# Kernel tuning notes

Hardware: AMD Instinct MI355X
Metric: run time of the kernel (lower is better)

Reference implementation:

```python
import jax, jax.numpy as jnp
import numpy as np
from jax import lax

L, B, S, D, H = 2, 8, 2048, 1024, 1024
LOG_H0 = float(np.log(0.5))  # h0 = g(0) = 0.5


def _log_g(x):
    # log of g(x) = x + 0.5 if x >= 0 else sigmoid(x)
    return jnp.where(x >= 0, jnp.log(jnp.where(x >= 0, x + 0.5, 1.0)), -jax.nn.softplus(-x))


def _mingru_layer(x, Wz, bz, Wh, bh):
    # x: (B,S,D) -> (B,S,H) via log-space heinsen associative scan
    k = jnp.einsum('bsd,hd->bsh', x, Wz) + bz          # gate pre-activation
    log_z = -jax.nn.softplus(-k)                        # log sigmoid(k)
    log_coeffs = -jax.nn.softplus(k)                    # log (1 - sigmoid(k))
    pre_h = jnp.einsum('bsd,hd->bsh', x, Wh) + bh
    log_values = log_z + _log_g(pre_h)                  # log(z * h_tilde)
    Bq = x.shape[0]
    # prepend initial state: coeff 0 (log 1), value log(h0)
    log_coeffs = jnp.pad(log_coeffs, ((0, 0), (1, 0), (0, 0)))
    log_values = jnp.concatenate(
        [jnp.full((Bq, 1, log_values.shape[-1]), LOG_H0, dtype=log_values.dtype), log_values], axis=1)
    a_star = jnp.cumsum(log_coeffs, axis=1)
    log_h = a_star + lax.cumlogsumexp(log_values - a_star, axis=1)
    return jnp.exp(log_h)[:, 1:]


def setup_inputs() -> dict:
    key = jax.random.key(0)
    ks = jax.random.split(key, 5)
    stdv = 1.0 / np.sqrt(D)
    u = lambda k, shp: jax.random.uniform(k, shp, jnp.float32, -stdv, stdv)
    return {
        'x': jax.random.normal(ks[0], (B, S, D), jnp.float32),
        'Wz': u(ks[1], (L, H, D)),
        'bz': u(ks[2], (L, H)),
        'Wh': u(ks[3], (L, H, D)),
        'bh': u(ks[4], (L, H)),
    }


def reference(x, Wz, bz, Wh, bh):
    h = x
    for l in range(Wz.shape[0]):
        h = _mingru_layer(h, Wz[l], bz[l], Wh[l], bh[l])
    return h  # (B,S,H), last layer outputs
```

## Files before the change

### kernel.cpp

```cpp
#include <hip/hip_runtime.h>
#include <hip/hip_bf16.h>


#define L_ 2
#define B_ 8
#define S_ 2048
#define D_ 1024
#define H_ 1024
#define M_ (B_*S_)
#define NC 32
#define CL (S_/NC)

typedef __bf16    bf16x8 __attribute__((ext_vector_type(8)));
typedef float     f32x4  __attribute__((ext_vector_type(4)));
typedef _Float16  h2     __attribute__((ext_vector_type(2)));
typedef _Float16  h4     __attribute__((ext_vector_type(4)));

__device__ __forceinline__ ushort f2bf(float f) {
    union { __hip_bfloat16 h; ushort u; } c;
    c.h = __float2bfloat16(f);
    return c.u;
}

__device__ __forceinline__ void async16(const void* g, void* l) {
    __builtin_amdgcn_global_load_lds(
        (const __attribute__((address_space(1))) unsigned int*)g,
        (__attribute__((address_space(3))) unsigned int*)l, 16, 0, 0);
}

__global__ __launch_bounds__(256) void cast_f32_bf16(const float* __restrict__ in,
                                                     ushort* __restrict__ out, int n4) {
    int i = blockIdx.x * 256 + threadIdx.x;
    if (i >= n4) return;
    float4 v = ((const float4*)in)[i];
    ushort4 o;
    o.x = f2bf(v.x); o.y = f2bf(v.y); o.z = f2bf(v.z); o.w = f2bf(v.w);
    ((ushort4*)out)[i] = o;
}

#define SWZ(R, c) (((R) << 6) + ((((c) ^ ((R) & 7))) << 3))

__global__ __launch_bounds__(256) void gemm_fused(const ushort* __restrict__ A,
                                                  const ushort* __restrict__ Wz,
                                                  const ushort* __restrict__ Wh,
                                                  const float* __restrict__ bz,
                                                  const float* __restrict__ bh,
                                                  h2* __restrict__ cv,
                                                  float* __restrict__ Ac,
                                                  float* __restrict__ Bc)
{
    __shared__ __align__(16) ushort sm[16384];
    ushort* As = sm;
    ushort* Zs = sm + 8192;
    ushort* Hs = sm + 12288;

    const int t    = threadIdx.x;
    const int lane = t & 63;
    const int wave = t >> 6;
    const int xcd = (int)blockIdx.x & 7;
    const int k8  = (int)blockIdx.x >> 3;
    const int nblk = k8 & 15;
    const int mblk = ((k8 >> 4) << 3) + xcd;
    const int m0 = mblk * 128;
    const int n0 = nblk * 64;
    const int wm = (wave >> 1) * 64;
    const int wn = (wave & 1) * 32;

    const int srow   = lane >> 3;
    const int scol_g = (((lane & 7) ^ srow) << 3);

    f32x4 accz[4][2] = {};
    f32x4 acch[4][2] = {};
    const int lrow = lane & 15;
    const int lcq  = lane >> 4;

    for (int kb = 0; kb < D_; kb += 64) {
        __syncthreads();
        #pragma unroll
        for (int i = 0; i < 4; ++i) {
            int r = i*32 + wave*8;
            async16(&A[(size_t)(m0 + r + srow)*D_ + kb + scol_g], &As[r*64]);
        }
        #pragma unroll
        for (int i = 0; i < 2; ++i) {
            int r = i*32 + wave*8;
            async16(&Wz[(size_t)(n0 + r + srow)*D_ + kb + scol_g], &Zs[r*64]);
            async16(&Wh[(size_t)(n0 + r + srow)*D_ + kb + scol_g], &Hs[r*64]);
        }
        __syncthreads();
        #pragma unroll
        for (int kk = 0; kk < 64; kk += 32) {
            const int cq = (kk >> 3) + lcq;
            bf16x8 af[4];
            #pragma unroll
            for (int mt = 0; mt < 4; ++mt) {
                int R = wm + mt*16 + lrow;
                uint4 u = *(const uint4*)&As[SWZ(R, cq)];
                af[mt] = __builtin_bit_cast(bf16x8, u);
            }
            #pragma unroll
            for (int nt = 0; nt < 2; ++nt) {
                int R = wn + nt*16 + lrow;
                uint4 uz = *(const uint4*)&Zs[SWZ(R, cq)];
                uint4 uh = *(const uint4*)&Hs[SWZ(R, cq)];
                bf16x8 zb = __builtin_bit_cast(bf16x8, uz);
                bf16x8 hb = __builtin_bit_cast(bf16x8, uh);
                #pragma unroll
                for (int mt = 0; mt < 4; ++mt) {
                    accz[mt][nt] = __builtin_amdgcn_mfma_f32_16x16x32_bf16(af[mt], zb, accz[mt][nt], 0, 0, 0);
                    acch[mt][nt] = __builtin_amdgcn_mfma_f32_16x16x32_bf16(af[mt], hb, acch[mt][nt], 0, 0, 0);
                }
            }
        }
    }

    __syncthreads();
    float2* seg = (float2*)sm;

    const int colq = lane & 15;
    const int rowq = (lane >> 4) * 4;
    #pragma unroll
    for (int nt = 0; nt < 2; ++nt) {
        const int n = n0 + wn + nt*16 + colq;
        const float bzv = bz[n];
        const float bhv = bh[n];
        #pragma unroll
        for (int mt = 0; mt < 4; ++mt) {
            float a = 1.f, bb = 0.f;
            #pragma unroll
            for (int r = 0; r < 4; ++r) {
                const int m = m0 + wm + mt*16 + rowq + r;
                float k = accz[mt][nt][r] + bzv;
                float p = acch[mt][nt][r] + bhv;
                float e   = __expf(-fabsf(k));
                float inv = 1.0f / (1.0f + e);
                float z   = (k >= 0.f) ? inv     : e * inv;
                float c   = (k >= 0.f) ? e * inv : inv;
                float g;
                if (p >= 0.f) g = p + 0.5f;
                else { float eg = __expf(p); g = eg / (1.0f + eg); }
                float v = z * g;
                h2 hv; hv[0] = (_Float16)c; hv[1] = (_Float16)v;
                cv[(size_t)m * H_ + n] = hv;
                bb = fmaf(c, bb, v);
                a *= c;
            }
            const int sidx = (wm >> 2) + mt*4 + (rowq >> 2);
            seg[sidx*65 + wn + nt*16 + colq] = make_float2(a, bb);
        }
    }
    __syncthreads();
    if (t < 128) {
        const int col  = t & 63;
        const int half = t >> 6;
        float a = 1.f, bb = 0.f;
        #pragma unroll
        for (int s = 0; s < 16; ++s) {
            float2 e = seg[(half*16 + s)*65 + col];
            bb = fmaf(e.x, bb, e.y);
            a *= e.x;
        }
        const int b     = m0 >> 11;
        const int chunk = ((m0 >> 6) & (NC - 1)) + half;
        const int q = (b*NC + chunk)*H_ + n0 + col;
        Ac[q] = a; Bc[q] = bb;
    }
}

__global__ __launch_bounds__(256) void scan_chunk_combine(const float* __restrict__ Ac,
                                                          const float* __restrict__ Bc,
                                                          float* __restrict__ hin)
{
    int q = blockIdx.x * 256 + threadIdx.x;
    int h = q & (H_-1);
    int b = q >> 10;
    float hcur = 0.5f;
    #pragma unroll
    for (int c = 0; c < NC; ++c) {
        int idx = (b*NC + c)*H_ + h;
        hin[idx] = hcur;
        hcur = fmaf(Ac[idx], hcur, Bc[idx]);
    }
}

__global__ __launch_bounds__(256) void scan_emit(const h2* __restrict__ cv,
                                                 const float* __restrict__ hin,
                                                 float* __restrict__ outf,
                                                 ushort* __restrict__ outb,
                                                 const int write_bf16)
{
    int q = blockIdx.x * 256 + threadIdx.x;
    int hp = (q & 511) * 2;
    int c = (q >> 9) & (NC-1);
    int b = q >> 14;
    size_t base = (size_t)(b*S_ + c*CL) * H_ + hp;
    int qh = (b*NC + c)*H_ + hp;
    float h0 = hin[qh], h1 = hin[qh + 1];
    if (write_bf16) {
        #pragma unroll 4
        for (int tt = 0; tt < CL; ++tt) {
            h4 e = *(const h4*)&cv[base + (size_t)tt * H_];
            h0 = fmaf((float)e[0], h0, (float)e[1]);
            h1 = fmaf((float)e[2], h1, (float)e[3]);
            ushort2 o; o.x = f2bf(h0); o.y = f2bf(h1);
            *(ushort2*)&outb[base + (size_t)tt * H_] = o;
        }
    } else {
        #pragma unroll 4
        for (int tt = 0; tt < CL; ++tt) {
            h4 e = *(const h4*)&cv[base + (size_t)tt * H_];
            h0 = fmaf((float)e[0], h0, (float)e[1]);
            h1 = fmaf((float)e[2], h1, (float)e[3]);
            *(float2*)&outf[base + (size_t)tt * H_] = make_float2(h0, h1);
        }
    }
}

extern "C" void kernel_launch(void* const* d_in, const int* in_sizes, int n_in,
                              void* d_out, int out_size, void* d_ws, size_t ws_size,
                              hipStream_t stream)
{
    const float* x  = (const float*)d_in[0];
    const float* Wz = (const float*)d_in[1];
    const float* bz = (const float*)d_in[2];
    const float* Wh = (const float*)d_in[3];
    const float* bh = (const float*)d_in[4];
    float* out = (float*)d_out;

    ushort* xb  = (ushort*)d_ws;
    ushort* wzb = xb  + (size_t)M_*D_;
    ushort* whb = wzb + (size_t)L_*H_*D_;
    h2*     cv  = (h2*)(whb + (size_t)L_*H_*D_);
    float*  Ac  = (float*)(cv + (size_t)M_*H_);
    float*  Bc  = Ac + B_*NC*H_;
    float*  hin = Bc + B_*NC*H_;

    cast_f32_bf16<<<(M_*D_/4)/256, 256, 0, stream>>>(x, xb, M_*D_/4);
    cast_f32_bf16<<<(L_*H_*D_/4)/256, 256, 0, stream>>>(Wz, wzb, L_*H_*D_/4);
    cast_f32_bf16<<<(L_*H_*D_/4)/256, 256, 0, stream>>>(Wh, whb, L_*H_*D_/4);

    const int gemm_grid = (M_/128) * (H_/64);
    for (int l = 0; l < L_; ++l) {
        gemm_fused<<<gemm_grid, 256, 0, stream>>>(xb,
                                                  wzb + (size_t)l*H_*D_,
                                                  whb + (size_t)l*H_*D_,
                                                  bz + l*H_, bh + l*H_,
                                                  cv, Ac, Bc);
        scan_chunk_combine<<<(B_*H_)/256, 256, 0, stream>>>(Ac, Bc, hin);
        scan_emit<<<(B_*NC*H_/2)/256, 256, 0, stream>>>(cv, hin, out, xb, (l == 0) ? 1 : 0);
    }
}
```

Before: 340.9 us.

## Enlarge fused GEMM tile and software-pipeline async LDS loads with double buffering

The fused gate/candidate GEMM now uses 256x128 tiles with 512 threads and 128KB of dynamic LDS split into two buffers. Async global-to-LDS loads for the next K step are issued in four phases between MFMA groups, with explicit vmcnt waits, barriers and s_setprio. The aim is to overlap memory traffic with matrix math and raise reuse per loaded byte. In exchange it brings higher register pressure, lower occupancy and fragile hand-tuned waitcnt ordering. The epilogue chunk reduction is widened to match the larger tile.

New measurement: 335.4 us. No clear change (-1.6%).

```diff
diff --git a/kernel.cpp b/kernel.cpp
--- a/kernel.cpp
+++ b/kernel.cpp
@@ -39,103 +39,168 @@
 }
 
 #define SWZ(R, c) (((R) << 6) + ((((c) ^ ((R) & 7))) << 3))
-
-__global__ __launch_bounds__(256) void gemm_fused(const ushort* __restrict__ A,
-                                                  const ushort* __restrict__ Wz,
-                                                  const ushort* __restrict__ Wh,
-                                                  const float* __restrict__ bz,
-                                                  const float* __restrict__ bh,
-                                                  h2* __restrict__ cv,
-                                                  float* __restrict__ Ac,
-                                                  float* __restrict__ Bc)
+#define MFMA16 __builtin_amdgcn_mfma_f32_16x16x32_bf16
+#define FENCE() asm volatile("" ::: "memory")
+
+__global__ __launch_bounds__(512, 2) void gemm_fused(const ushort* __restrict__ A,
+                                                     const ushort* __restrict__ Wz,
+                                                     const ushort* __restrict__ Wh,
+                                                     const float* __restrict__ bz,
+                                                     const float* __restrict__ bh,
+                                                     h2* __restrict__ cv,
+                                                     float* __restrict__ Ac,
+                                                     float* __restrict__ Bc)
 {
-    __shared__ __align__(16) ushort sm[16384];
-    ushort* As = sm;
-    ushort* Zs = sm + 8192;
-    ushort* Hs = sm + 12288;
-
-    const int t    = threadIdx.x;
-    const int lane = t & 63;
-    const int wave = t >> 6;
-    const int xcd = (int)blockIdx.x & 7;
-    const int k8  = (int)blockIdx.x >> 3;
-    const int nblk = k8 & 15;
-    const int mblk = ((k8 >> 4) << 3) + xcd;
-    const int m0 = mblk * 128;
-    const int n0 = nblk * 64;
-    const int wm = (wave >> 1) * 64;
-    const int wn = (wave & 1) * 32;
-
-    const int srow   = lane >> 3;
-    const int scol_g = (((lane & 7) ^ srow) << 3);
-
-    f32x4 accz[4][2] = {};
-    f32x4 acch[4][2] = {};
+    extern __shared__ __align__(16) ushort sm[];
+
+    const int tid  = threadIdx.x;
+    const int lane = tid & 63;
+    const int wave = tid >> 6;
+    const int bid  = (int)blockIdx.x;
+    const int xcd  = bid & 7;
+    const int k8   = bid >> 3;
+    const int nblk = k8 & 7;
+    const int mblk = ((k8 >> 3) << 3) + xcd;
+    const int m0 = mblk << 8;
+    const int n0 = nblk << 7;
+    const int wm = (wave >> 2) << 7;
+    const int wn = (wave & 3) << 5;
     const int lrow = lane & 15;
     const int lcq  = lane >> 4;
 
-    for (int kb = 0; kb < D_; kb += 64) {
-        __syncthreads();
-        #pragma unroll
-        for (int i = 0; i < 4; ++i) {
-            int r = i*32 + wave*8;
-            async16(&A[(size_t)(m0 + r + srow)*D_ + kb + scol_g], &As[r*64]);
-        }
-        #pragma unroll
-        for (int i = 0; i < 2; ++i) {
-            int r = i*32 + wave*8;
-            async16(&Wz[(size_t)(n0 + r + srow)*D_ + kb + scol_g], &Zs[r*64]);
-            async16(&Wh[(size_t)(n0 + r + srow)*D_ + kb + scol_g], &Hs[r*64]);
-        }
-        __syncthreads();
-        #pragma unroll
-        for (int kk = 0; kk < 64; kk += 32) {
-            const int cq = (kk >> 3) + lcq;
-            bf16x8 af[4];
-            #pragma unroll
-            for (int mt = 0; mt < 4; ++mt) {
-                int R = wm + mt*16 + lrow;
-                uint4 u = *(const uint4*)&As[SWZ(R, cq)];
-                af[mt] = __builtin_bit_cast(bf16x8, u);
-            }
-            #pragma unroll
-            for (int nt = 0; nt < 2; ++nt) {
-                int R = wn + nt*16 + lrow;
-                uint4 uz = *(const uint4*)&Zs[SWZ(R, cq)];
-                uint4 uh = *(const uint4*)&Hs[SWZ(R, cq)];
-                bf16x8 zb = __builtin_bit_cast(bf16x8, uz);
-                bf16x8 hb = __builtin_bit_cast(bf16x8, uh);
+    const int e0 = tid, e1 = tid + 512;
+    const int r0 = e0 >> 3, c0 = (((e0 & 7) ^ (r0 & 7)) << 3);
+    const int r1 = e1 >> 3, c1 = (((e1 & 7) ^ (r1 & 7)) << 3);
+    const uint offA0  = (uint)((m0 + r0) * D_ + c0);
+    const uint offA0b = (uint)((m0 + r1) * D_ + c1);
+    const uint offA1  = offA0  + (uint)(128 * D_);
+    const uint offA1b = offA0b + (uint)(128 * D_);
+    const uint offW0  = (uint)((n0 + r0) * D_ + c0);
+    const uint offW0b = (uint)((n0 + r1) * D_ + c1);
+    const int dj0 = wave << 9;
+    const int dj1 = 4096 + (wave << 9);
+
+    f32x4 accz[8][2] = {};
+    f32x4 acch[8][2] = {};
+
+    async16(A  + offA0,  &sm[dj0]);
+    async16(A  + offA0b, &sm[dj1]);
+    async16(A  + offA1,  &sm[8192  + dj0]);
+    async16(A  + offA1b, &sm[8192  + dj1]);
+    async16(Wz + offW0,  &sm[16384 + dj0]);
+    async16(Wz + offW0b, &sm[16384 + dj1]);
+    async16(Wh + offW0,  &sm[24576 + dj0]);
+    async16(Wh + offW0b, &sm[24576 + dj1]);
+
+    #pragma unroll 2
+    for (int t = 0; t < 16; ++t) {
+        const int cur = (t & 1) << 15;
+        const int nxt = cur ^ 32768;
+        const uint kbn = (uint)((t < 15 ? t + 1 : 15) << 6);
+        bf16x8 a0[4][2], a1[4][2], zf[2][2], hf[2][2];
+
+        asm volatile("s_waitcnt vmcnt(2)" ::: "memory");
+        __builtin_amdgcn_s_barrier();
+        FENCE();
+        #pragma unroll
+        for (int mt = 0; mt < 4; ++mt)
+            #pragma unroll
+            for (int kk = 0; kk < 2; ++kk)
+                a0[mt][kk] = *(const bf16x8*)&sm[cur + SWZ(wm + mt*16 + lrow, kk*4 + lcq)];
+        #pragma unroll
+        for (int nt = 0; nt < 2; ++nt)
+            #pragma unroll
+            for (int kk = 0; kk < 2; ++kk)
+                zf[nt][kk] = *(const bf16x8*)&sm[cur + 16384 + SWZ(wn + nt*16 + lrow, kk*4 + lcq)];
+        async16(A + offA0  + kbn, &sm[nxt + dj0]);
+        async16(A + offA0b + kbn, &sm[nxt + dj1]);
+        __builtin_amdgcn_s_setprio(1);
+        #pragma unroll
+        for (int kk = 0; kk < 2; ++kk)
+            #pragma unroll
+            for (int nt = 0; nt < 2; ++nt)
                 #pragma unroll
-                for (int mt = 0; mt < 4; ++mt) {
-                    accz[mt][nt] = __builtin_amdgcn_mfma_f32_16x16x32_bf16(af[mt], zb, accz[mt][nt], 0, 0, 0);
-                    acch[mt][nt] = __builtin_amdgcn_mfma_f32_16x16x32_bf16(af[mt], hb, acch[mt][nt], 0, 0, 0);
-                }
-            }
-        }
-    }
-
+                for (int mt = 0; mt < 4; ++mt)
+                    accz[mt][nt] = MFMA16(a0[mt][kk], zf[nt][kk], accz[mt][nt], 0, 0, 0);
+        __builtin_amdgcn_s_setprio(0);
+
+        __builtin_amdgcn_s_barrier();
+        FENCE();
+        #pragma unroll
+        for (int mt = 0; mt < 4; ++mt)
+            #pragma unroll
+            for (int kk = 0; kk < 2; ++kk)
+                a1[mt][kk] = *(const bf16x8*)&sm[cur + SWZ(wm + 64 + mt*16 + lrow, kk*4 + lcq)];
+        async16(A + offA1  + kbn, &sm[nxt + 8192 + dj0]);
+        async16(A + offA1b + kbn, &sm[nxt + 8192 + dj1]);
+        __builtin_amdgcn_s_setprio(1);
+        #pragma unroll
+        for (int kk = 0; kk < 2; ++kk)
+            #pragma unroll
+            for (int nt = 0; nt < 2; ++nt)
+                #pragma unroll
+                for (int mt = 0; mt < 4; ++mt)
+                    accz[4 + mt][nt] = MFMA16(a1[mt][kk], zf[nt][kk], accz[4 + mt][nt], 0, 0, 0);
+        __builtin_amdgcn_s_setprio(0);
+
+        asm volatile("s_waitcnt vmcnt(4)" ::: "memory");
+        __builtin_amdgcn_s_barrier();
+        FENCE();
+        #pragma unroll
+        for (int nt = 0; nt < 2; ++nt)
+            #pragma unroll
+            for (int kk = 0; kk < 2; ++kk)
+                hf[nt][kk] = *(const bf16x8*)&sm[cur + 24576 + SWZ(wn + nt*16 + lrow, kk*4 + lcq)];
+        async16(Wz + offW0  + kbn, &sm[nxt + 16384 + dj0]);
+        async16(Wz + offW0b + kbn, &sm[nxt + 16384 + dj1]);
+        __builtin_amdgcn_s_setprio(1);
+        #pragma unroll
+        for (int kk = 0; kk < 2; ++kk)
+            #pragma unroll
+            for (int nt = 0; nt < 2; ++nt)
+                #pragma unroll
+                for (int mt = 0; mt < 4; ++mt)
+                    acch[4 + mt][nt] = MFMA16(a1[mt][kk], hf[nt][kk], acch[4 + mt][nt], 0, 0, 0);
+        __builtin_amdgcn_s_setprio(0);
+
+        __builtin_amdgcn_s_barrier();
+        FENCE();
+        async16(Wh + offW0  + kbn, &sm[nxt + 24576 + dj0]);
+        async16(Wh + offW0b + kbn, &sm[nxt + 24576 + dj1]);
+        __builtin_amdgcn_s_setprio(1);
+        #pragma unroll
+        for (int kk = 0; kk < 2; ++kk)
+            #pragma unroll
+            for (int nt = 0; nt < 2; ++nt)
+                #pragma unroll
+                for (int mt = 0; mt < 4; ++mt)
+                    acch[mt][nt] = MFMA16(a0[mt][kk], hf[nt][kk], acch[mt][nt], 0, 0, 0);
+        __builtin_amdgcn_s_setprio(0);
+    }
+
+    asm volatile("s_waitcnt vmcnt(0)" ::: "memory");
     __syncthreads();
+
     float2* seg = (float2*)sm;
-
     const int colq = lane & 15;
-    const int rowq = (lane >> 4) * 4;
+    const int rowq = (lane >> 4) << 2;
     #pragma unroll
     for (int nt = 0; nt < 2; ++nt) {
         const int n = n0 + wn + nt*16 + colq;
         const float bzv = bz[n];
         const float bhv = bh[n];
         #pragma unroll
-        for (int mt = 0; mt < 4; ++mt) {
+        for (int mt = 0; mt < 8; ++mt) {
             float a = 1.f, bb = 0.f;
             #pragma unroll
             for (int r = 0; r < 4; ++r) {
                 const int m = m0 + wm + mt*16 + rowq + r;
-                float k = accz[mt][nt][r] + bzv;
-                float p = acch[mt][nt][r] + bhv;
-                float e   = __expf(-fabsf(k));
+                float kx = accz[mt][nt][r] + bzv;
+                float p  = acch[mt][nt][r] + bhv;
+                float e   = __expf(-fabsf(kx));
                 float inv = 1.0f / (1.0f + e);
-                float z   = (k >= 0.f) ? inv     : e * inv;
-                float c   = (k >= 0.f) ? e * inv : inv;
+                float z   = (kx >= 0.f) ? inv     : e * inv;
+                float c   = (kx >= 0.f) ? e * inv : inv;
                 float g;
                 if (p >= 0.f) g = p + 0.5f;
                 else { float eg = __expf(p); g = eg / (1.0f + eg); }
@@ -146,22 +211,22 @@
                 a *= c;
             }
             const int sidx = (wm >> 2) + mt*4 + (rowq >> 2);
-            seg[sidx*65 + wn + nt*16 + colq] = make_float2(a, bb);
+            seg[sidx*130 + wn + nt*16 + colq] = make_float2(a, bb);
         }
     }
     __syncthreads();
-    if (t < 128) {
-        const int col  = t & 63;
-        const int half = t >> 6;
+    {
+        const int col = tid & 127;
+        const int ch  = tid >> 7;
         float a = 1.f, bb = 0.f;
         #pragma unroll
         for (int s = 0; s < 16; ++s) {
-            float2 e = seg[(half*16 + s)*65 + col];
-            bb = fmaf(e.x, bb, e.y);
-            a *= e.x;
+            float2 e2 = seg[(ch*16 + s)*130 + col];
+            bb = fmaf(e2.x, bb, e2.y);
+            a *= e2.x;
         }
         const int b     = m0 >> 11;
-        const int chunk = ((m0 >> 6) & (NC - 1)) + half;
+        const int chunk = ((m0 >> 6) & (NC - 1)) + ch;
         const int q = (b*NC + chunk)*H_ + n0 + col;
         Ac[q] = a; Bc[q] = bb;
     }
@@ -227,6 +292,13 @@
     const float* bh = (const float*)d_in[4];
     float* out = (float*)d_out;
 
+    static bool attr_set = false;
+    if (!attr_set) {
+        (void)hipFuncSetAttribute(reinterpret_cast<const void*>(gemm_fused),
+                                  hipFuncAttributeMaxDynamicSharedMemorySize, 131072);
+        attr_set = true;
+    }
+
     ushort* xb  = (ushort*)d_ws;
     ushort* wzb = xb  + (size_t)M_*D_;
     ushort* whb = wzb + (size_t)L_*H_*D_;
@@ -239,13 +311,13 @@
     cast_f32_bf16<<<(L_*H_*D_/4)/256, 256, 0, stream>>>(Wz, wzb, L_*H_*D_/4);
     cast_f32_bf16<<<(L_*H_*D_/4)/256, 256, 0, stream>>>(Wh, whb, L_*H_*D_/4);
 
-    const int gemm_grid = (M_/128) * (H_/64);
+    const int gemm_grid = (M_/256) * (H_/128);
     for (int l = 0; l < L_; ++l) {
-        gemm_fused<<<gemm_grid, 256, 0, stream>>>(xb,
-                                                  wzb + (size_t)l*H_*D_,
-                                                  whb + (size_t)l*H_*D_,
-                                                  bz + l*H_, bh + l*H_,
-                                                  cv, Ac, Bc);
+        gemm_fused<<<gemm_grid, 512, 131072, stream>>>(xb,
+                                                       wzb + (size_t)l*H_*D_,
+                                                       whb + (size_t)l*H_*D_,
+                                                       bz + l*H_, bh + l*H_,
+                                                       cv, Ac, Bc);
         scan_chunk_combine<<<(B_*H_)/256, 256, 0, stream>>>(Ac, Bc, hin);
         scan_emit<<<(B_*NC*H_/2)/256, 256, 0, stream>>>(cv, hin, out, xb, (l == 0) ? 1 : 0);
     }
```
